# Kernel tuning notes

Measured on AMD Instinct MI355X. Metric: run time of the kernel, lower is better.

## Reference

```python
import jax, jax.numpy as jnp
import numpy as np
import math

B, S, DIM = 2, 2048, 2048
H, KV, HD = 16, 1, 128  # query heads, kv heads, head dim


def setup_inputs() -> dict:
    key = jax.random.key(0)
    ks = jax.random.split(key, 6)
    std = 0.02
    return {
        "hidden_states": jax.random.normal(ks[0], (B, S, DIM), jnp.float32),
        "attention_mask": jnp.zeros((B, 1, S, S), jnp.float32),
        "wq": jax.random.normal(ks[1], (DIM, H * HD), jnp.float32) * std,
        "bq": jnp.zeros((H * HD,), jnp.float32),
        "wk": jax.random.normal(ks[2], (DIM, KV * HD), jnp.float32) * std,
        "bk": jnp.zeros((KV * HD,), jnp.float32),
        "wv": jax.random.normal(ks[3], (DIM, KV * HD), jnp.float32) * std,
        "bv": jnp.zeros((KV * HD,), jnp.float32),
        "wo": jax.random.normal(ks[4], (H * HD, DIM), jnp.float32) * std,
        "bo": jnp.zeros((DIM,), jnp.float32),
    }


def reference(hidden_states, attention_mask, wq, bq, wk, bk, wv, bv, wo, bo):
    b, s, _ = hidden_states.shape
    q = (hidden_states @ wq + bq).reshape(b, s, H, HD)
    k = (hidden_states @ wk + bk).reshape(b, s, KV, HD)
    v = (hidden_states @ wv + bv).reshape(b, s, KV, HD)
    # [b, h, s, d]
    q = jnp.transpose(q, (0, 2, 1, 3))
    k = jnp.transpose(k, (0, 2, 1, 3))
    v = jnp.transpose(v, (0, 2, 1, 3))
    # broadcast shared KV heads to all query heads (num_kv_heads < num_query_heads)
    repeats = H // KV
    k = jnp.repeat(k, repeats, axis=1)
    v = jnp.repeat(v, repeats, axis=1)
    scores = jnp.einsum('bhqd,bhkd->bhqk', q, k) / math.sqrt(HD)
    scores = scores + attention_mask
    weights = jax.nn.softmax(scores, axis=-1)
    attn = jnp.einsum('bhqk,bhkd->bhqd', weights, v)
    attn = jnp.transpose(attn, (0, 2, 1, 3)).reshape(b, s, H * HD)
    return attn @ wo + bo
```

## Files before the change

kernel.cpp:

```cpp
#include <hip/hip_runtime.h>
#include <hip/hip_bf16.h>
#include <stdint.h>

#define S_LEN 2048
#define DIMSZ 2048
#define NH    16
#define HD    128
#define NQK   2176
#define NQKV  2304
#define NT2   (S_LEN / 128)

typedef short  bf16x8  __attribute__((ext_vector_type(8)));
typedef float  floatx4 __attribute__((ext_vector_type(4)));
typedef float  floatx16 __attribute__((ext_vector_type(16)));
typedef int    intx4   __attribute__((ext_vector_type(4)));
typedef unsigned short u16;

#define mfma32 __builtin_amdgcn_mfma_f32_32x32x16_bf16
#define LOG2E 1.4426950408889634f

__device__ __forceinline__ u16 f2bf(float x) {
  unsigned int u = __builtin_bit_cast(unsigned int, x);
  u = (u + 0x7FFFu + ((u >> 16) & 1u)) >> 16;
  return (u16)u;
}
__device__ __forceinline__ float bf2f(unsigned int bits) {
  return __builtin_bit_cast(float, bits << 16);
}

__device__ __forceinline__ int cvtpk(float lo, float hi) {
  int r;
  asm("v_cvt_pk_bf16_f32 %0, %1, %2" : "=v"(r) : "v"(lo), "v"(hi));
  return r;
}

#if __has_builtin(__builtin_amdgcn_exp2f)
__device__ __forceinline__ float fexp2(float x) { return __builtin_amdgcn_exp2f(x); }
#else
__device__ __forceinline__ float fexp2(float x) { return exp2f(x); }
#endif

#if __has_builtin(__builtin_amdgcn_permlane32_swap)
__device__ __forceinline__ void half_swap(int& a, int& b) {
  auto r = __builtin_amdgcn_permlane32_swap(a, b, false, false);
  a = (int)r[0]; b = (int)r[1];
}
__device__ __forceinline__ float red_max32(float x) {
  int xi = __builtin_bit_cast(int, x);
  auto r = __builtin_amdgcn_permlane32_swap(xi, xi, false, false);
  return fmaxf(__builtin_bit_cast(float, (int)r[0]), __builtin_bit_cast(float, (int)r[1]));
}
__device__ __forceinline__ float red_add32(float x) {
  int xi = __builtin_bit_cast(int, x);
  auto r = __builtin_amdgcn_permlane32_swap(xi, xi, false, false);
  return __builtin_bit_cast(float, (int)r[0]) + __builtin_bit_cast(float, (int)r[1]);
}
#else
__device__ __forceinline__ void half_swap(int& a, int& b) {
  int as = __shfl_xor(a, 32);
  int bs = __shfl_xor(b, 32);
  int lane = threadIdx.x & 63;
  int na = (lane < 32) ? a : bs;
  int nb = (lane < 32) ? as : b;
  a = na; b = nb;
}
__device__ __forceinline__ float red_max32(float x) { return fmaxf(x, __shfl_xor(x, 32)); }
__device__ __forceinline__ float red_add32(float x) { return x + __shfl_xor(x, 32); }
#endif

__device__ __forceinline__ void gload16(const void* g, void* l) {
  __builtin_amdgcn_global_load_lds(
      reinterpret_cast<const __attribute__((address_space(1))) void*>(reinterpret_cast<uintptr_t>(g)),
      reinterpret_cast<__attribute__((address_space(3))) void*>(reinterpret_cast<uintptr_t>(l)),
      16, 0, 0);
}

__global__ void k_cvt_bf16(const float* __restrict__ in, u16* __restrict__ out, int n4) {
  int i = blockIdx.x * blockDim.x + threadIdx.x;
  if (i < n4) {
    float4 v = ((const float4*)in)[i];
    ushort4 o;
    o.x = f2bf(v.x); o.y = f2bf(v.y); o.z = f2bf(v.z); o.w = f2bf(v.w);
    ((ushort4*)out)[i] = o;
  }
}

__global__ void k_transpose_bf16(const float* __restrict__ in, u16* __restrict__ out,
                                 int K, int N, int rowOff) {
  __shared__ float t[64][65];
  int c0 = blockIdx.x * 64;
  int r0 = blockIdx.y * 64;
  int tid = threadIdx.x;
  int lr = tid >> 6;
  int lc = tid & 63;
#pragma unroll
  for (int i = 0; i < 16; ++i) {
    int r = lr + i * 4;
    t[r][lc] = in[(size_t)(r0 + r) * N + c0 + lc];
  }
  __syncthreads();
#pragma unroll
  for (int i = 0; i < 16; ++i) {
    int r = lr + i * 4;
    out[(size_t)(rowOff + c0 + r) * K + r0 + lc] = f2bf(t[lc][r]);
  }
}

__global__ void k_bias_concat(const float* __restrict__ bq, const float* __restrict__ bk,
                              const float* __restrict__ bv, float* __restrict__ out) {
  int i = blockIdx.x * 256 + threadIdx.x;
  if (i < NQKV) out[i] = (i < 2048) ? bq[i] : (i < NQK ? bk[i - 2048] : bv[i - NQK]);
}

__device__ __forceinline__ void stage_tile(const u16* __restrict__ G, int ldg, int row0, int kt,
                                           u16* lbase, int wid, int lane) {
#pragma unroll
  for (int i = 0; i < 4; ++i) {
    int c   = (wid * 4 + i) * 64 + lane;
    int row = c >> 3, cin = c & 7;
    int cs  = cin ^ (row & 7);
    const u16* g = G + (size_t)(row0 + row) * ldg + kt * 64 + cs * 8;
    gload16(g, (char*)lbase + (wid * 4 + i) * 1024);
  }
}

template <int OMODE>
__global__ __launch_bounds__(256)
void k_gemm(const u16* __restrict__ A, const u16* __restrict__ Bt,
            const float* __restrict__ bias, void* __restrict__ Cout,
            u16* __restrict__ vt, int M, int N, int K) {
  __shared__ u16 lA[2][128 * 64];
  __shared__ u16 lB[2][128 * 64];
  const int tid = threadIdx.x, lane = tid & 63, wid = tid >> 6;
  const int wm = wid >> 1, wn = wid & 1;
  const int tmN = M >> 7;
  const int nwg = tmN * (N >> 7);
  const int qx = nwg >> 3;
  const int swz = (blockIdx.x & 7) * qx + (blockIdx.x >> 3);
  const int tm = swz % tmN, tn = swz / tmN;
  const int nk = K >> 6;

  stage_tile(A, K, tm * 128, 0, lA[0], wid, lane);
  stage_tile(Bt, K, tn * 128, 0, lB[0], wid, lane);
  __syncthreads();

  floatx4 acc[4][4] = {};
  int buf = 0;
  for (int kt = 0; kt < nk; ++kt) {
    if (kt + 1 < nk) {
      stage_tile(A, K, tm * 128, kt + 1, lA[buf ^ 1], wid, lane);
      stage_tile(Bt, K, tn * 128, kt + 1, lB[buf ^ 1], wid, lane);
    }
    const char* pa = (const char*)&lA[buf][0];
    const char* pb = (const char*)&lB[buf][0];
#pragma unroll
    for (int kk = 0; kk < 2; ++kk) {
      bf16x8 af[4], bfr[4];
      int gch = kk * 4 + (lane >> 4);
#pragma unroll
      for (int f = 0; f < 4; ++f) {
        int ra = wm * 64 + f * 16 + (lane & 15);
        af[f]  = *(const bf16x8*)(pa + ra * 128 + ((gch ^ (ra & 7)) << 4));
        int rb = wn * 64 + f * 16 + (lane & 15);
        bfr[f] = *(const bf16x8*)(pb + rb * 128 + ((gch ^ (rb & 7)) << 4));
      }
      __builtin_amdgcn_s_setprio(1);
#pragma unroll
      for (int fm = 0; fm < 4; ++fm)
#pragma unroll
        for (int fn = 0; fn < 4; ++fn)
          acc[fm][fn] = __builtin_amdgcn_mfma_f32_16x16x32_bf16(af[fm], bfr[fn], acc[fm][fn], 0, 0, 0);
      __builtin_amdgcn_s_setprio(0);
    }
    __syncthreads();
    buf ^= 1;
  }

#pragma unroll
  for (int fm = 0; fm < 4; ++fm)
#pragma unroll
    for (int fn = 0; fn < 4; ++fn)
#pragma unroll
      for (int r = 0; r < 4; ++r) {
        int rowg = tm * 128 + wm * 64 + fm * 16 + (lane >> 4) * 4 + r;
        int colg = tn * 128 + wn * 64 + fn * 16 + (lane & 15);
        float v = acc[fm][fn][r] + bias[colg];
        if constexpr (OMODE == 1) {
          ((float*)Cout)[(size_t)rowg * N + colg] = v;
        } else {
          if (colg < NQK) {
            ((u16*)Cout)[(size_t)rowg * N + colg] = f2bf(v);
          } else {
            int d = colg - NQK;
            int bg = rowg >> 11, s = rowg & 2047;
            vt[((size_t)bg * HD + d) * S_LEN + s] = f2bf(v);
          }
        }
      }
}

__device__ __forceinline__ void stage_kv128(const u16* __restrict__ qkv, const u16* __restrict__ vt,
                                            int b, int kt, u16* lK, u16* lV, int wid, int lane) {
#pragma unroll
  for (int i = 0; i < 4; ++i) {
    int seg = wid * 4 + i;
    int r = seg * 4 + (lane >> 4);
    int cin = lane & 15;
    int cs = cin ^ (r & 7);
    const u16* gk = qkv + (size_t)(b * S_LEN + kt * 128 + r) * NQKV + 2048 + cs * 8;
    gload16(gk, (char*)lK + seg * 1024);
    const u16* gv = vt + ((size_t)b * HD + r) * S_LEN + kt * 128 + cs * 8;
    gload16(gv, (char*)lV + seg * 1024);
  }
}

__device__ __forceinline__ void mask_write128(u16* lMb, int mq, int mc, floatx4 m0, floatx4 m1) {
  intx4 w;
  w[0] = cvtpk(m0[0] * LOG2E, m0[1] * LOG2E);
  w[1] = cvtpk(m0[2] * LOG2E, m0[3] * LOG2E);
  w[2] = cvtpk(m1[0] * LOG2E, m1[1] * LOG2E);
  w[3] = cvtpk(m1[2] * LOG2E, m1[3] * LOG2E);
  *(intx4*)((char*)lMb + mq * 256 + ((mc ^ (mq & 7)) << 4)) = w;
}

__global__ __launch_bounds__(512)
void k_attn(const u16* __restrict__ qkv, const u16* __restrict__ vt,
            const float* __restrict__ mask, u16* __restrict__ attn) {
  __shared__ __align__(16) u16 lK[2][128 * 128];
  __shared__ __align__(16) u16 lV[2][128 * 128];
  __shared__ __align__(16) u16 lMb[2][32 * 128];
  const int tid = threadIdx.x, lane = tid & 63, wid = tid >> 6;
  const int qt = blockIdx.x, hg = blockIdx.y, b = blockIdx.z;
  const int h = hg * 8 + wid;
  const int q = lane & 31, h5 = lane >> 5;
  const float c_sl2 = 0.08838834764831845f * LOG2E;

  bf16x8 qf[8];
  const size_t qrow = (size_t)(b * S_LEN + qt * 32 + q);
#pragma unroll
  for (int cs = 0; cs < 8; ++cs)
    qf[cs] = *(const bf16x8*)(qkv + qrow * NQKV + h * HD + cs * 16 + h5 * 8);

  const int qb = q * 256;
  int offK[8], offVc[8];
#pragma unroll
  for (int cs = 0; cs < 8; ++cs)
    offK[cs] = qb + (((cs * 2 + h5) ^ (q & 7)) << 4);
#pragma unroll
  for (int hf = 0; hf < 2; ++hf)
#pragma unroll
    for (int ks = 0; ks < 4; ++ks)
      offVc[hf * 4 + ks] = (((hf * 8 + ks * 2 + h5) ^ (q & 7)) << 4);

  float m_ = -1e30f, l_ = 0.f;
  floatx16 acco[4] = {};

  const int mq = tid >> 4, mc = tid & 15;
  const float* mrow = mask + (size_t)b * S_LEN * S_LEN + (size_t)(qt * 32 + mq) * S_LEN + mc * 8;

  stage_kv128(qkv, vt, b, 0, lK[0], lV[0], wid, lane);
  {
    floatx4 m0 = *(const floatx4*)(mrow);
    floatx4 m1 = *(const floatx4*)(mrow + 4);
    mask_write128(&lMb[0][0], mq, mc, m0, m1);
  }
  __syncthreads();

  int buf = 0;
  for (int kt = 0; kt < NT2; ++kt) {
    floatx4 mr0, mr1;
    if (kt + 1 < NT2) {
      stage_kv128(qkv, vt, b, kt + 1, lK[buf ^ 1], lV[buf ^ 1], wid, lane);
      mr0 = *(const floatx4*)(mrow + (size_t)(kt + 1) * 128);
      mr1 = *(const floatx4*)(mrow + (size_t)(kt + 1) * 128 + 4);
    }
    const char* pKb = (const char*)&lK[buf][0];
    const char* pVb = (const char*)&lV[buf][0];
    const char* pMb = (const char*)&lMb[buf][0];

#pragma unroll
    for (int hf = 0; hf < 2; ++hf) {
      floatx16 accs0 = {}, accs1 = {};
      const char* pK = pKb + hf * 16384;
      __builtin_amdgcn_s_setprio(1);
#pragma unroll
      for (int cs = 0; cs < 8; ++cs) {
        bf16x8 kf0 = *(const bf16x8*)(pK + offK[cs]);
        bf16x8 kf1 = *(const bf16x8*)(pK + 8192 + offK[cs]);
        accs0 = mfma32(kf0, qf[cs], accs0, 0, 0, 0);
        accs1 = mfma32(kf1, qf[cs], accs1, 0, 0, 0);
      }
      __builtin_amdgcn_s_setprio(0);

      float pr[32];
      float pm0 = -1e30f, pm1 = -1e30f, pm2 = -1e30f, pm3 = -1e30f;
#pragma unroll
      for (int kb = 0; kb < 2; ++kb)
#pragma unroll
        for (int rg = 0; rg < 4; ++rg) {
          ushort4 mu = *(const ushort4*)(pMb + qb +
                         (((hf * 8 + kb * 4 + rg) ^ (q & 7)) << 4) + h5 * 8);
          float s0 = (kb ? accs1[rg * 4 + 0] : accs0[rg * 4 + 0]) * c_sl2 + bf2f(mu.x);
          float s1 = (kb ? accs1[rg * 4 + 1] : accs0[rg * 4 + 1]) * c_sl2 + bf2f(mu.y);
          float s2 = (kb ? accs1[rg * 4 + 2] : accs0[rg * 4 + 2]) * c_sl2 + bf2f(mu.z);
          float s3 = (kb ? accs1[rg * 4 + 3] : accs0[rg * 4 + 3]) * c_sl2 + bf2f(mu.w);
          pr[kb * 16 + rg * 4 + 0] = s0; pm0 = fmaxf(pm0, s0);
          pr[kb * 16 + rg * 4 + 1] = s1; pm1 = fmaxf(pm1, s1);
          pr[kb * 16 + rg * 4 + 2] = s2; pm2 = fmaxf(pm2, s2);
          pr[kb * 16 + rg * 4 + 3] = s3; pm3 = fmaxf(pm3, s3);
        }
      float rowm = red_max32(fmaxf(fmaxf(pm0, pm1), fmaxf(pm2, pm3)));

      if (__any(rowm > m_ + 11.5415603f)) {
        float mn = fmaxf(m_, rowm);
        float al = fexp2(m_ - mn);
        m_ = mn;
        l_ *= al;
#pragma unroll
        for (int dt = 0; dt < 4; ++dt) acco[dt] *= al;
      }
      float ps0 = 0.f, ps1 = 0.f, ps2 = 0.f, ps3 = 0.f;
#pragma unroll
      for (int j = 0; j < 32; j += 4) {
        float e0 = fexp2(pr[j + 0] - m_); pr[j + 0] = e0; ps0 += e0;
        float e1 = fexp2(pr[j + 1] - m_); pr[j + 1] = e1; ps1 += e1;
        float e2 = fexp2(pr[j + 2] - m_); pr[j + 2] = e2; ps2 += e2;
        float e3 = fexp2(pr[j + 3] - m_); pr[j + 3] = e3; ps3 += e3;
      }
      l_ += red_add32((ps0 + ps1) + (ps2 + ps3));

      bf16x8 pf[4];
#pragma unroll
      for (int kb = 0; kb < 2; ++kb)
#pragma unroll
        for (int s = 0; s < 2; ++s) {
          int base = kb * 16 + s * 8;
          int A0 = cvtpk(pr[base + 0], pr[base + 1]);
          int A1 = cvtpk(pr[base + 2], pr[base + 3]);
          int B0 = cvtpk(pr[base + 4], pr[base + 5]);
          int B1 = cvtpk(pr[base + 6], pr[base + 7]);
          half_swap(A0, B0);
          half_swap(A1, B1);
          intx4 w;
          w[0] = A0; w[1] = A1; w[2] = B0; w[3] = B1;
          pf[kb * 2 + s] = __builtin_bit_cast(bf16x8, w);
        }

      __builtin_amdgcn_s_setprio(1);
#pragma unroll
      for (int dt = 0; dt < 4; ++dt)
#pragma unroll
        for (int ks = 0; ks < 4; ++ks) {
          bf16x8 vf = *(const bf16x8*)(pVb + dt * 8192 + qb + offVc[hf * 4 + ks]);
          acco[dt] = mfma32(vf, pf[ks], acco[dt], 0, 0, 0);
        }
      __builtin_amdgcn_s_setprio(0);
    }

    if (kt + 1 < NT2)
      mask_write128(&lMb[buf ^ 1][0], mq, mc, mr0, mr1);
    __syncthreads();
    buf ^= 1;
  }

  float inv = 1.0f / l_;
  u16* obase = attn + qrow * DIMSZ + h * HD;
#pragma unroll
  for (int dt = 0; dt < 4; ++dt)
#pragma unroll
    for (int rg = 0; rg < 4; ++rg) {
      int d0 = dt * 32 + rg * 8 + h5 * 4;
      ushort4 st;
      st.x = f2bf(acco[dt][rg * 4 + 0] * inv);
      st.y = f2bf(acco[dt][rg * 4 + 1] * inv);
      st.z = f2bf(acco[dt][rg * 4 + 2] * inv);
      st.w = f2bf(acco[dt][rg * 4 + 3] * inv);
      *(ushort4*)(obase + d0) = st;
    }
}

extern "C" void kernel_launch(void* const* d_in, const int* in_sizes, int n_in,
                              void* d_out, int out_size, void* d_ws, size_t ws_size,
                              hipStream_t stream) {
  const float* hidden = (const float*)d_in[0];
  const float* mask   = (const float*)d_in[1];
  const float* wq = (const float*)d_in[2];
  const float* bq = (const float*)d_in[3];
  const float* wk = (const float*)d_in[4];
  const float* bk = (const float*)d_in[5];
  const float* wv = (const float*)d_in[6];
  const float* bv = (const float*)d_in[7];
  const float* wo = (const float*)d_in[8];
  const float* bo = (const float*)d_in[9];
  float* out = (float*)d_out;

  char* ws = (char*)d_ws;
  u16*   hb    = (u16*)(ws);
  u16*   wqkvT = (u16*)(ws + 16777216);
  u16*   woT   = (u16*)(ws + 26214400);
  float* bqkv  = (float*)(ws + 34603008);
  u16*   qkv   = (u16*)(ws + 34612224);
  u16*   vt    = (u16*)(ws + 53486592);
  u16*   attn  = (u16*)(ws + 54535168);

  k_cvt_bf16<<<dim3(8192), dim3(256), 0, stream>>>(hidden, hb, 4096 * 2048 / 4);
  k_transpose_bf16<<<dim3(32, 32), dim3(256), 0, stream>>>(wq, wqkvT, 2048, 2048, 0);
  k_transpose_bf16<<<dim3(2, 32),  dim3(256), 0, stream>>>(wk, wqkvT, 2048, 128, 2048);
  k_transpose_bf16<<<dim3(2, 32),  dim3(256), 0, stream>>>(wv, wqkvT, 2048, 128, NQK);
  k_transpose_bf16<<<dim3(32, 32), dim3(256), 0, stream>>>(wo, woT, 2048, 2048, 0);
  k_bias_concat<<<dim3(9), dim3(256), 0, stream>>>(bq, bk, bv, bqkv);

  k_gemm<0><<<dim3(576), dim3(256), 0, stream>>>(hb, wqkvT, bqkv, (void*)qkv, vt, 4096, NQKV, 2048);
  k_attn<<<dim3(64, 2, 2), dim3(512), 0, stream>>>(qkv, vt, mask, attn);
  k_gemm<1><<<dim3(512), dim3(256), 0, stream>>>(attn, woT, bo, (void*)out, (u16*)nullptr, 4096, 2048, 2048);
}
```

Baseline: 213.7 us.

## Merge QKV weight transposes, drop GEMM block swizzle, widen LDS XOR swizzle

Replaces the three separate Q/K/V weight-transpose launches with one combined kernel, which saves two launches. The GEMM now takes its tile coordinates straight from a 2D grid instead of the XCD-aware 1D swizzle. The attention kernel's LDS XOR swizzle for K, V and the mask buffer is widened from 3 bits to 4 bits so bank conflicts on 256-byte rows drop. Mask LDS offsets are also precomputed into registers. Removing the swizzle may hurt L2 locality across XCDs, and the extra offset registers add register pressure.

```diff
diff --git a/kernel.cpp b/kernel.cpp
--- a/kernel.cpp
+++ b/kernel.cpp
@@ -85,8 +85,34 @@
   }
 }
 
+__global__ void k_transpose_qkv(const float* __restrict__ wq, const float* __restrict__ wk,
+                                const float* __restrict__ wv, u16* __restrict__ out, int K) {
+  __shared__ float t[64][65];
+  int orow0 = blockIdx.x * 64;
+  int r0 = blockIdx.y * 64;
+  const float* src;
+  int N, scol0;
+  if (orow0 < 2048)      { src = wq; N = 2048; scol0 = orow0; }
+  else if (orow0 < NQK)  { src = wk; N = 128;  scol0 = orow0 - 2048; }
+  else                   { src = wv; N = 128;  scol0 = orow0 - NQK; }
+  int tid = threadIdx.x;
+  int lr = tid >> 6;
+  int lc = tid & 63;
+#pragma unroll
+  for (int i = 0; i < 16; ++i) {
+    int r = lr + i * 4;
+    t[r][lc] = src[(size_t)(r0 + r) * N + scol0 + lc];
+  }
+  __syncthreads();
+#pragma unroll
+  for (int i = 0; i < 16; ++i) {
+    int r = lr + i * 4;
+    out[(size_t)(orow0 + r) * K + r0 + lc] = f2bf(t[lc][r]);
+  }
+}
+
 __global__ void k_transpose_bf16(const float* __restrict__ in, u16* __restrict__ out,
-                                 int K, int N, int rowOff) {
+                                 int K, int N) {
   __shared__ float t[64][65];
   int c0 = blockIdx.x * 64;
   int r0 = blockIdx.y * 64;
@@ -102,7 +128,7 @@
 #pragma unroll
   for (int i = 0; i < 16; ++i) {
     int r = lr + i * 4;
-    out[(size_t)(rowOff + c0 + r) * K + r0 + lc] = f2bf(t[lc][r]);
+    out[(size_t)(c0 + r) * K + r0 + lc] = f2bf(t[lc][r]);
   }
 }
 
@@ -133,11 +159,7 @@
   __shared__ u16 lB[2][128 * 64];
   const int tid = threadIdx.x, lane = tid & 63, wid = tid >> 6;
   const int wm = wid >> 1, wn = wid & 1;
-  const int tmN = M >> 7;
-  const int nwg = tmN * (N >> 7);
-  const int qx = nwg >> 3;
-  const int swz = (blockIdx.x & 7) * qx + (blockIdx.x >> 3);
-  const int tm = swz % tmN, tn = swz / tmN;
+  const int tm = blockIdx.x, tn = blockIdx.y;
   const int nk = K >> 6;
 
   stage_tile(A, K, tm * 128, 0, lA[0], wid, lane);
@@ -206,7 +228,7 @@
     int seg = wid * 4 + i;
     int r = seg * 4 + (lane >> 4);
     int cin = lane & 15;
-    int cs = cin ^ (r & 7);
+    int cs = cin ^ (r & 15);
     const u16* gk = qkv + (size_t)(b * S_LEN + kt * 128 + r) * NQKV + 2048 + cs * 8;
     gload16(gk, (char*)lK + seg * 1024);
     const u16* gv = vt + ((size_t)b * HD + r) * S_LEN + kt * 128 + cs * 8;
@@ -220,7 +242,7 @@
   w[1] = cvtpk(m0[2] * LOG2E, m0[3] * LOG2E);
   w[2] = cvtpk(m1[0] * LOG2E, m1[1] * LOG2E);
   w[3] = cvtpk(m1[2] * LOG2E, m1[3] * LOG2E);
-  *(intx4*)((char*)lMb + mq * 256 + ((mc ^ (mq & 7)) << 4)) = w;
+  *(intx4*)((char*)lMb + mq * 256 + ((mc ^ (mq & 15)) << 4)) = w;
 }
 
 __global__ __launch_bounds__(512)
@@ -242,15 +264,18 @@
     qf[cs] = *(const bf16x8*)(qkv + qrow * NQKV + h * HD + cs * 16 + h5 * 8);
 
   const int qb = q * 256;
-  int offK[8], offVc[8];
+  int offK[8], offVc[8], offM[16];
 #pragma unroll
   for (int cs = 0; cs < 8; ++cs)
-    offK[cs] = qb + (((cs * 2 + h5) ^ (q & 7)) << 4);
+    offK[cs] = qb + (((cs * 2 + h5) ^ (q & 15)) << 4);
 #pragma unroll
   for (int hf = 0; hf < 2; ++hf)
 #pragma unroll
     for (int ks = 0; ks < 4; ++ks)
-      offVc[hf * 4 + ks] = (((hf * 8 + ks * 2 + h5) ^ (q & 7)) << 4);
+      offVc[hf * 4 + ks] = (((hf * 8 + ks * 2 + h5) ^ (q & 15)) << 4);
+#pragma unroll
+  for (int c = 0; c < 16; ++c)
+    offM[c] = qb + ((c ^ (q & 15)) << 4) + h5 * 8;
 
   float m_ = -1e30f, l_ = 0.f;
   floatx16 acco[4] = {};
@@ -298,8 +323,7 @@
       for (int kb = 0; kb < 2; ++kb)
 #pragma unroll
         for (int rg = 0; rg < 4; ++rg) {
-          ushort4 mu = *(const ushort4*)(pMb + qb +
-                         (((hf * 8 + kb * 4 + rg) ^ (q & 7)) << 4) + h5 * 8);
+          ushort4 mu = *(const ushort4*)(pMb + offM[hf * 8 + kb * 4 + rg]);
           float s0 = (kb ? accs1[rg * 4 + 0] : accs0[rg * 4 + 0]) * c_sl2 + bf2f(mu.x);
           float s1 = (kb ? accs1[rg * 4 + 1] : accs0[rg * 4 + 1]) * c_sl2 + bf2f(mu.y);
           float s2 = (kb ? accs1[rg * 4 + 2] : accs0[rg * 4 + 2]) * c_sl2 + bf2f(mu.z);
@@ -404,13 +428,11 @@
   u16*   attn  = (u16*)(ws + 54535168);
 
   k_cvt_bf16<<<dim3(8192), dim3(256), 0, stream>>>(hidden, hb, 4096 * 2048 / 4);
-  k_transpose_bf16<<<dim3(32, 32), dim3(256), 0, stream>>>(wq, wqkvT, 2048, 2048, 0);
-  k_transpose_bf16<<<dim3(2, 32),  dim3(256), 0, stream>>>(wk, wqkvT, 2048, 128, 2048);
-  k_transpose_bf16<<<dim3(2, 32),  dim3(256), 0, stream>>>(wv, wqkvT, 2048, 128, NQK);
-  k_transpose_bf16<<<dim3(32, 32), dim3(256), 0, stream>>>(wo, woT, 2048, 2048, 0);
+  k_transpose_qkv<<<dim3(36, 32), dim3(256), 0, stream>>>(wq, wk, wv, wqkvT, 2048);
+  k_transpose_bf16<<<dim3(32, 32), dim3(256), 0, stream>>>(wo, woT, 2048, 2048);
   k_bias_concat<<<dim3(9), dim3(256), 0, stream>>>(bq, bk, bv, bqkv);
 
-  k_gemm<0><<<dim3(576), dim3(256), 0, stream>>>(hb, wqkvT, bqkv, (void*)qkv, vt, 4096, NQKV, 2048);
+  k_gemm<0><<<dim3(32, 18), dim3(256), 0, stream>>>(hb, wqkvT, bqkv, (void*)qkv, vt, 4096, NQKV, 2048);
   k_attn<<<dim3(64, 2, 2), dim3(512), 0, stream>>>(qkv, vt, mask, attn);
-  k_gemm<1><<<dim3(512), dim3(256), 0, stream>>>(attn, woT, bo, (void*)out, (u16*)nullptr, 4096, 2048, 2048);
-}
+  k_gemm<1><<<dim3(32, 16), dim3(256), 0, stream>>>(attn, woT, bo, (void*)out, (u16*)nullptr, 4096, 2048, 2048);
+}
```

Result: faster. 199.7 us (-6.6%).
